# Kernel optimization log

Hardware: AMD Instinct MI355X
Metric: run time of the kernel (lower is better)

## Reference

```python
import jax, jax.numpy as jnp
import numpy as np


def _to_complex(x):
    # trailing axis holds (real, imag)
    return x[..., 0] + 1j * x[..., 1]


def _nufft2c(img, omega, csm):
    """Exact type-2 non-uniform DFT with coil sensitivities (reference for nufft2c_torch).

    img:   (H, W) real or complex image
    omega: (2, M) k-space coords in cycles/pixel, in [-0.5, 0.5]
    csm:   (C, H, W) complex coil sensitivity maps
    returns (C, M) complex k-space, centered & orthonormal-style 1/sqrt(HW) scaling.
    """
    H, W = img.shape
    y = jnp.arange(H, dtype=jnp.float32) - H / 2.0  # centered pixel coords
    z = jnp.arange(W, dtype=jnp.float32) - W / 2.0
    ey = jnp.exp(-2j * jnp.pi * omega[0][:, None] * y[None, :])  # (M, H)
    ez = jnp.exp(-2j * jnp.pi * omega[1][:, None] * z[None, :])  # (M, W)
    sim = csm * img[None, :, :].astype(csm.dtype)                # (C, H, W)
    tmp = jnp.einsum('chw,mw->cmh', sim, ez)                     # (C, M, H)
    k = jnp.einsum('cmh,mh->cm', tmp, ey) / np.float32(np.sqrt(H * W))
    return k


def setup_inputs() -> dict:
    key = jax.random.key(0)
    k0, k1, k2, k3, k4 = jax.random.split(key, 5)
    H = W = 300
    C = 4       # coils
    M = 4096    # non-Cartesian k-space samples
    img_pred = jax.random.normal(k0, (H, W, 1), jnp.float32)
    kdata = jax.random.normal(k1, (1, C, M, 2), jnp.float32)
    all_omega = jax.random.uniform(k2, (1, 2, M), jnp.float32) - 0.5  # cycles/pixel
    all_dcomp = jax.random.uniform(k3, (1, M), jnp.float32)
    all_csm = jax.random.normal(k4, (C, H, W, 2), jnp.float32)
    return {
        'img_pred': img_pred,
        'kdata': kdata,
        'all_omega': all_omega,
        'all_dcomp': all_dcomp,
        'all_csm': all_csm,
    }


def reference(img_pred, kdata, all_omega, all_dcomp, all_csm):
    Ncontrast = 1
    csm = _to_complex(all_csm)   # (C, H, W)
    kd = _to_complex(kdata)      # (Ncontrast, C, M)
    two_pi = jnp.float32(2.0 * np.pi)
    # radial k-space weighting, (Ncontrast, M)
    weight = jnp.sqrt((all_omega[:, 0, :] * two_pi) ** 2 +
                      (all_omega[:, 1, :] * two_pi) ** 2) + 1.0
    loss = jnp.float32(0.0)
    for ii in range(Ncontrast):
        img = img_pred[:, :, ii]                       # (H, W)
        ksp = _nufft2c(img, all_omega[ii], csm)        # (C, M)
        d = weight[ii][None, :] * (ksp - kd[ii])       # weighted complex residual
        # MSELoss over view_as_real == mean over all real & imag components
        loss = loss + jnp.mean(jnp.stack([d.real, d.imag]) ** 2)
    return loss
```

## Files before the change

kernel.cpp:

```cpp
#include <hip/hip_runtime.h>
#include <math.h>

#define HH 300
#define WW 300
#define CC 4
#define MM 4096
#define KP 640
#define NKC (KP/32)
#define CSTRIDE 384
#define MP (CC*CSTRIDE)
#define NP 8192
#define NRB (MP/128)

#define ABLK 1920
#define BBLK 2560
#define ZBLK 129

typedef __attribute__((ext_vector_type(4))) float f32x4;
typedef __attribute__((ext_vector_type(4))) int int4v;
typedef __attribute__((ext_vector_type(8))) int int8v;

#define TWO_PI 6.283185307179586f

__device__ __forceinline__ size_t cmaddr(int R, int row, int k) {
    return ((size_t)(k >> 5) * R + row) * 32 + (k & 31);
}

__device__ __forceinline__ float aval(const float* img, const float* csm,
                                      int c, int h, int k) {
    if (k >= 2 * WW) return 0.0f;
    int w = (k < WW) ? k : k - WW;
    float im = img[h * WW + w];
    const float* cs = csm + (((size_t)c * HH + h) * WW + w) * 2;
    return ((k < WW) ? cs[0] : cs[1]) * im;
}

__global__ __launch_bounds__(256) void prep_kernel(
    const float* __restrict__ img, const float* __restrict__ csm,
    const float* __restrict__ omega, unsigned char* __restrict__ A,
    unsigned char* __restrict__ B, float* __restrict__ Kz,
    int* __restrict__ counters, float* __restrict__ out)
{
    const int bid = blockIdx.x;
    if (bid == 0 && threadIdx.x == 0) out[0] = 0.0f;
    if (bid < ABLK) {
        int idx = bid * 256 + threadIdx.x;
        int row = idx / (KP / 2);
        int k   = (idx - row * (KP / 2)) * 2;
        int c = row / CSTRIDE;
        int h = row - c * CSTRIDE;
        float v0 = 0.0f, v1 = 0.0f;
        if (h < HH) { v0 = aval(img, csm, c, h, k); v1 = aval(img, csm, c, h, k + 1); }
        int pk = __builtin_amdgcn_cvt_pk_fp8_f32(v0, v1, 0, false);
        *(ushort*)(A + cmaddr(MP, row, k)) = (ushort)pk;
    } else if (bid < ABLK + BBLK) {
        int idx = (bid - ABLK) * 256 + threadIdx.x;
        int m  = idx / 160;
        int wp = idx - m * 160;
        if (wp < 150) {
            int w = wp * 2;
            float om1 = omega[MM + m];
            float a0 = TWO_PI * om1 * (float)(w - 150);
            float a1 = TWO_PI * om1 * (float)(w - 149);
            float s0 = __sinf(a0), c0 = __cosf(a0);
            float s1 = __sinf(a1), c1 = __cosf(a1);
            ushort rr = (ushort)__builtin_amdgcn_cvt_pk_fp8_f32(c0, c1, 0, false);
            ushort ii = (ushort)__builtin_amdgcn_cvt_pk_fp8_f32(-s0, -s1, 0, false);
            ushort ni = (ushort)__builtin_amdgcn_cvt_pk_fp8_f32(s0, s1, 0, false);
            *(ushort*)(B + cmaddr(NP, m,      w))        = rr;
            *(ushort*)(B + cmaddr(NP, m,      WW + w))   = ni;
            *(ushort*)(B + cmaddr(NP, m + MM, w))        = ii;
            *(ushort*)(B + cmaddr(NP, m + MM, WW + w))   = rr;
        } else {
            int k = 600 + (wp - 150) * 4;
            *(unsigned int*)(B + cmaddr(NP, m,      k)) = 0u;
            *(unsigned int*)(B + cmaddr(NP, m + MM, k)) = 0u;
        }
    } else {
        int idx = (bid - ABLK - BBLK) * 256 + threadIdx.x;
        if (idx < 2 * CC * MM)           Kz[idx] = 0.0f;
        else if (idx < 2 * CC * MM + 32) counters[idx - 2 * CC * MM] = 0;
    }
}

__global__ __launch_bounds__(256) void gemm_kernel(
    const unsigned char* __restrict__ A, const unsigned char* __restrict__ B,
    const float* __restrict__ omega, const float* __restrict__ kdata,
    float* __restrict__ Kacc, int* __restrict__ counters,
    float* __restrict__ out)
{
    __shared__ float2 red[128];
    __shared__ int winner;
    __shared__ float lred[4];

    const int t    = threadIdx.x;
    const int wave = t >> 6;
    const int ln   = t & 63;

    const int flat = blockIdx.x;
    const int xcd  = flat & 7;
    const int q    = flat >> 3;
    const int cb   = xcd * 8 + (q & 7);
    const int rowb = q >> 3;
    const int row0 = rowb * 128;
    const int col0 = cb * 128;

    const int wr = wave >> 1, wc = wave & 1;
    const int lr = ln & 15;
    const int lq = ln >> 4;

    if (t < 128) red[t] = make_float2(0.0f, 0.0f);

    const int arow = row0 + wr * 64 + lr;
    const int bcol = col0 + wc * 64 + lr;

    f32x4 acc[4][4] = {};

    #pragma unroll
    for (int kc = 0; kc < NKC; kc += 4) {
        int8v a[4], b[4];
        #pragma unroll
        for (int i = 0; i < 4; ++i) {
            const unsigned char* pA = A + ((size_t)(kc + lq) * MP + arow + i * 16) * 32;
            int4v lo = *(const int4v*)pA;
            int4v hi = *(const int4v*)(pA + 16);
            a[i] = __builtin_shufflevector(lo, hi, 0, 1, 2, 3, 4, 5, 6, 7);
        }
        #pragma unroll
        for (int j = 0; j < 4; ++j) {
            const unsigned char* pB = B + ((size_t)(kc + lq) * NP + bcol + j * 16) * 32;
            int4v lo = *(const int4v*)pB;
            int4v hi = *(const int4v*)(pB + 16);
            b[j] = __builtin_shufflevector(lo, hi, 0, 1, 2, 3, 4, 5, 6, 7);
        }
        #pragma unroll
        for (int i = 0; i < 4; ++i)
            #pragma unroll
            for (int j = 0; j < 4; ++j)
                acc[i][j] = __builtin_amdgcn_mfma_scale_f32_16x16x128_f8f6f4(
                    a[i], b[j], acc[i][j], 0, 0,
                    0, 0x7f7f7f7f, 0, 0x7f7f7f7f);
    }

    __syncthreads();

    const int c  = row0 / CSTRIDE;
    const int h0 = row0 - c * CSTRIDE;

    #pragma unroll
    for (int j = 0; j < 4; ++j) {
        const int jcol = wc * 64 + j * 16 + lr;
        const int m = (col0 + jcol) & (MM - 1);
        const float om0 = omega[m];
        const float th = TWO_PI * om0;
        const float ss = __sinf(th), sc = __cosf(th);
        const float str = sc, sti = -ss;
        float s2r = str * str - sti * sti, s2i = 2.0f * str * sti;
        float s4r = s2r * s2r - s2i * s2i, s4i = 2.0f * s2r * s2i;
        float s8r = s4r * s4r - s4i * s4i, s8i = 2.0f * s4r * s4i;
        float s16r = s8r * s8r - s8i * s8i, s16i = 2.0f * s8r * s8i;

        const int hb0 = h0 + wr * 64 + lq * 4;
        const float thb = TWO_PI * om0 * (float)(hb0 - 150);
        const float sn = __sinf(thb), cs = __cosf(thb);
        float byr = cs, byi = -sn;

        float pr = 0.0f, pi = 0.0f;
        #pragma unroll
        for (int i = 0; i < 4; ++i) {
            float er = byr, ei = byi;
            #pragma unroll
            for (int r = 0; r < 4; ++r) {
                const float v = acc[i][j][r];
                pr = fmaf(v, er, pr);
                pi = fmaf(v, ei, pi);
                float nr = er * str - ei * sti;
                ei = er * sti + ei * str;
                er = nr;
            }
            float nbr = byr * s16r - byi * s16i;
            byi = byr * s16i + byi * s16r;
            byr = nbr;
        }
        pr += __shfl_down(pr, 32); pi += __shfl_down(pi, 32);
        pr += __shfl_down(pr, 16); pi += __shfl_down(pi, 16);
        if (lq == 0) {
            atomicAdd(&red[jcol].x, pr);
            atomicAdd(&red[jcol].y, pi);
        }
    }
    __syncthreads();

    const int g = (col0 >> 7) & 31;
    const bool realcol = (col0 < MM);
    if (t < 128) {
        const float2 p = red[t];
        const int m = (col0 + t) & (MM - 1);
        float* kc = Kacc + ((size_t)c * MM + m) * 2;
        if (realcol) {
            atomicAdd(kc,     p.x);
            atomicAdd(kc + 1, p.y);
        } else {
            atomicAdd(kc,    -p.y);
            atomicAdd(kc + 1,  p.x);
        }
    }
    __syncthreads();
    if (t == 0) winner = (atomicAdd(&counters[g], 1) == 23) ? 1 : 0;
    __syncthreads();

    if (winner) {
        float val = 0.0f;
        #pragma unroll
        for (int u = 0; u < 2; ++u) {
            const int idx = u * 256 + t;
            const int c2 = idx >> 7;
            const int m  = g * 128 + (idx & 127);
            float* kc = Kacc + ((size_t)c2 * MM + m) * 2;
            float kr = atomicAdd(kc,     0.0f) * (1.0f / 300.0f);
            float ki = atomicAdd(kc + 1, 0.0f) * (1.0f / 300.0f);
            const float om0 = omega[m];
            const float om1 = omega[MM + m];
            const size_t kidx = ((size_t)c2 * MM + m) * 2;
            const float kdr = kdata[kidx];
            const float kdi = kdata[kidx + 1];
            const float w0 = om0 * TWO_PI, w1 = om1 * TWO_PI;
            const float wg = sqrtf(w0 * w0 + w1 * w1) + 1.0f;
            const float dr = wg * (kr - kdr);
            const float di = wg * (ki - kdi);
            val += (dr * dr + di * di) * (1.0f / (2.0f * CC * MM));
        }
        #pragma unroll
        for (int off = 32; off > 0; off >>= 1) val += __shfl_down(val, off);
        if (ln == 0) lred[wave] = val;
        __syncthreads();
        if (t == 0) atomicAdd(out, lred[0] + lred[1] + lred[2] + lred[3]);
    }
}

extern "C" void kernel_launch(void* const* d_in, const int* in_sizes, int n_in,
                              void* d_out, int out_size, void* d_ws, size_t ws_size,
                              hipStream_t stream) {
    const float* img   = (const float*)d_in[0];
    const float* kdata = (const float*)d_in[1];
    const float* omega = (const float*)d_in[2];
    const float* csm   = (const float*)d_in[4];
    float* out = (float*)d_out;

    unsigned char* Aws = (unsigned char*)d_ws;
    unsigned char* Bws = (unsigned char*)d_ws + (1u << 20);
    float* Kacc     = (float*)((char*)d_ws + (8u << 20));
    int*   counters = (int*)((char*)d_ws + (8u << 20) + (256u << 10));

    prep_kernel<<<ABLK + BBLK + ZBLK, 256, 0, stream>>>(
        img, csm, omega, Aws, Bws, Kacc, counters, out);
    gemm_kernel<<<(NP / 128) * NRB, 256, 0, stream>>>(
        Aws, Bws, omega, kdata, Kacc, counters, out);
}
```

Before: 86.47 us.

## Stage FP8 GEMM tiles through LDS via direct global-to-LDS loads

The GEMM kernel now copies each K-stage's A and B tiles into shared memory with global_load_lds, using an XOR swizzle on the 16-byte halves to avoid bank conflicts. Waves then read their MFMA fragments from LDS instead of issuing redundant global loads, since two waves share each A row block and each B column block. This removes duplicate global traffic but adds two barriers per stage and has no double buffering, so load latency is no longer overlapped with MFMA work. The loop is also no longer fully unrolled.

Measured after the change: 87.88 us. Within noise of the previous version (+1.6%).

```diff
diff --git a/kernel.cpp b/kernel.cpp
--- a/kernel.cpp
+++ b/kernel.cpp
@@ -33,6 +33,12 @@
     float im = img[h * WW + w];
     const float* cs = csm + (((size_t)c * HH + h) * WW + w) * 2;
     return ((k < WW) ? cs[0] : cs[1]) * im;
+}
+
+__device__ __forceinline__ void glds16(const unsigned char* g, unsigned char* l) {
+    __builtin_amdgcn_global_load_lds(
+        (const __attribute__((address_space(1))) unsigned int*)g,
+        (__attribute__((address_space(3))) unsigned int*)l, 16, 0, 0);
 }
 
 __global__ __launch_bounds__(256) void prep_kernel(
@@ -89,6 +95,8 @@
     float* __restrict__ Kacc, int* __restrict__ counters,
     float* __restrict__ out)
 {
+    __shared__ unsigned char ldsA[4 * 128 * 32];
+    __shared__ unsigned char ldsB[4 * 128 * 32];
     __shared__ float2 red[128];
     __shared__ int winner;
     __shared__ float lred[4];
@@ -111,26 +119,40 @@
 
     if (t < 128) red[t] = make_float2(0.0f, 0.0f);
 
-    const int arow = row0 + wr * 64 + lr;
-    const int bcol = col0 + wc * 64 + lr;
+    const int sr   = t >> 1;
+    const int sh16 = ((t & 1) ^ ((sr >> 2) & 1)) * 16;
+    const int h0   = (lr >> 2) & 1;
 
     f32x4 acc[4][4] = {};
 
-    #pragma unroll
-    for (int kc = 0; kc < NKC; kc += 4) {
+    for (int s = 0; s < 5; ++s) {
+        if (s > 0) __syncthreads();
+        #pragma unroll
+        for (int u = 0; u < 4; ++u) {
+            const unsigned char* gA =
+                A + (((size_t)(4 * s + u) * MP + row0 + sr) << 5) + sh16;
+            const unsigned char* gB =
+                B + (((size_t)(4 * s + u) * NP + col0 + sr) << 5) + sh16;
+            glds16(gA, ldsA + (u << 12) + (t << 4));
+            glds16(gB, ldsB + (u << 12) + (t << 4));
+        }
+        __syncthreads();
+
         int8v a[4], b[4];
         #pragma unroll
         for (int i = 0; i < 4; ++i) {
-            const unsigned char* pA = A + ((size_t)(kc + lq) * MP + arow + i * 16) * 32;
-            int4v lo = *(const int4v*)pA;
-            int4v hi = *(const int4v*)(pA + 16);
+            const int r = wr * 64 + i * 16 + lr;
+            const unsigned char* p = ldsA + (((lq << 7) + r) << 5);
+            int4v lo = *(const int4v*)(p + (h0 << 4));
+            int4v hi = *(const int4v*)(p + ((h0 ^ 1) << 4));
             a[i] = __builtin_shufflevector(lo, hi, 0, 1, 2, 3, 4, 5, 6, 7);
         }
         #pragma unroll
         for (int j = 0; j < 4; ++j) {
-            const unsigned char* pB = B + ((size_t)(kc + lq) * NP + bcol + j * 16) * 32;
-            int4v lo = *(const int4v*)pB;
-            int4v hi = *(const int4v*)(pB + 16);
+            const int r = wc * 64 + j * 16 + lr;
+            const unsigned char* p = ldsB + (((lq << 7) + r) << 5);
+            int4v lo = *(const int4v*)(p + (h0 << 4));
+            int4v hi = *(const int4v*)(p + ((h0 ^ 1) << 4));
             b[j] = __builtin_shufflevector(lo, hi, 0, 1, 2, 3, 4, 5, 6, 7);
         }
         #pragma unroll
@@ -142,10 +164,8 @@
                     0, 0x7f7f7f7f, 0, 0x7f7f7f7f);
     }
 
-    __syncthreads();
-
     const int c  = row0 / CSTRIDE;
-    const int h0 = row0 - c * CSTRIDE;
+    const int h0r = row0 - c * CSTRIDE;
 
     #pragma unroll
     for (int j = 0; j < 4; ++j) {
@@ -160,7 +180,7 @@
         float s8r = s4r * s4r - s4i * s4i, s8i = 2.0f * s4r * s4i;
         float s16r = s8r * s8r - s8i * s8i, s16i = 2.0f * s8r * s8i;
 
-        const int hb0 = h0 + wr * 64 + lq * 4;
+        const int hb0 = h0r + wr * 64 + lq * 4;
         const float thb = TWO_PI * om0 * (float)(hb0 - 150);
         const float sn = __sinf(thb), cs = __cosf(thb);
         float byr = cs, byi = -sn;
```
